# Kernel optimization log

Hardware: AMD Instinct MI355X
Metric: run time of the kernel (lower is better)

The kernel has to match this reference:

```python
import jax, jax.numpy as jnp
import numpy as np

N_NODES = 100000
N_EDGES = 600000
IN_SIZE = 128
OUT_SIZE = 128
N_GRAPHS = 100
BN_EPS = 1e-5


def setup_inputs() -> dict:
    key = jax.random.key(0)
    ks = jax.random.split(key, 8)
    h = jax.random.normal(ks[0], (N_NODES, IN_SIZE), dtype=jnp.float32)
    norm = jax.random.uniform(ks[1], (N_NODES, 1), dtype=jnp.float32)
    src = jax.random.randint(ks[2], (N_EDGES,), 0, N_NODES, dtype=jnp.int32)
    dst = jax.random.randint(ks[3], (N_EDGES,), 0, N_NODES, dtype=jnp.int32)
    graph_ids = jnp.sort(jax.random.randint(ks[4], (N_NODES,), 0, N_GRAPHS, dtype=jnp.int32))
    # Linear + BatchNorm params
    W = jax.random.normal(ks[5], (IN_SIZE, OUT_SIZE), dtype=jnp.float32) / np.sqrt(IN_SIZE)
    b = jnp.zeros((OUT_SIZE,), dtype=jnp.float32)
    gamma = jnp.ones((OUT_SIZE,), dtype=jnp.float32)
    beta = jnp.zeros((OUT_SIZE,), dtype=jnp.float32)
    return {"h": h, "norm": norm, "W": W, "b": b, "gamma": gamma, "beta": beta,
            "src": src, "dst": dst, "graph_ids": graph_ids}


def reference(h, norm, W, b, gamma, beta, src, dst, graph_ids):
    # pre-normalize, scatter-sum over edges (copy_src + sum), post-normalize
    x = h * norm                                            # [N, in]
    agg = jax.ops.segment_sum(x[src], dst, num_segments=N_NODES)  # SpMM
    x = agg * norm
    # linear + relu
    x = jax.nn.relu(jnp.dot(x, W) + b)                      # [N, out]
    # BatchNorm1d (training-mode: batch mean, biased variance)
    mean = jnp.mean(x, axis=0)
    var = jnp.mean(jnp.square(x - mean), axis=0)
    x = (x - mean) * jax.lax.rsqrt(var + BN_EPS) * gamma + beta
    # sum_nodes pooling per graph
    phis = jax.ops.segment_sum(x, graph_ids, num_segments=N_GRAPHS)  # [G, out]
    return (x, phis)
```

## Files before the change

kernel.cpp:

```cpp
#include <hip/hip_runtime.h>
#include <hip/hip_bf16.h>

#define N_NODES 100000
#define N_EDGES 600000
#define CH 128
#define N_GRAPHS 100
#define BN_EPS 1e-5f
#define NBUCKET 32
#define CAP 16
#define OVFCAP 8192
#define EDGE_BLOCKS 2344
#define GEMM_BLOCKS 1563
#define GATHER_BLOCKS 2048
#define BN_BLOCKS 1563
#define ZERO_INTS (N_NODES + 2 * NBUCKET * CH + 4)
#define ZERO_BLOCKS 423
#define PHIS_BLOCKS 50
#define WT_BLOCKS 64

typedef __bf16 bf16x8 __attribute__((ext_vector_type(8)));
typedef float f32x4 __attribute__((ext_vector_type(4)));

__device__ __forceinline__ ushort f2bf(float f) {
    union { float f; unsigned u; } x; x.f = f;
    unsigned u = x.u;
    unsigned r = (u + 0x7fffu + ((u >> 16) & 1u)) >> 16;
    return (ushort)r;
}
__device__ __forceinline__ float bflo(unsigned p) { return __builtin_bit_cast(float, p << 16); }
__device__ __forceinline__ float bfhi(unsigned p) { return __builtin_bit_cast(float, p & 0xffff0000u); }

__global__ __launch_bounds__(256) void k_prep(const float* __restrict__ W,
        int* __restrict__ zbase, ushort* __restrict__ Wt, float* __restrict__ phis) {
    unsigned bid = blockIdx.x;
    int tid = threadIdx.x;
    if (bid < ZERO_BLOCKS) {
        int i = bid * 256 + tid;
        if (i < ZERO_INTS) zbase[i] = 0;
    } else if (bid < ZERO_BLOCKS + PHIS_BLOCKS) {
        int i = (bid - ZERO_BLOCKS) * 256 + tid;
        phis[i] = 0.f;
    } else {
        int t = (bid - ZERO_BLOCKS - PHIS_BLOCKS) * 256 + tid;
        int k = t >> 7, o = t & 127;
        Wt[o * CH + k] = f2bf(W[t]);
    }
}

__global__ __launch_bounds__(256) void k_fill(const int* __restrict__ src,
        const int* __restrict__ dst, int* __restrict__ cnt,
        int* __restrict__ ovfcur, int* __restrict__ ovf, int* __restrict__ esrc) {
    int e = blockIdx.x * 256 + threadIdx.x;
    if (e < N_EDGES) {
        int d = dst[e], s = src[e];
        int slot = atomicAdd(&cnt[d], 1);
        if (slot < CAP) esrc[d * CAP + slot] = s;
        else { int p = atomicAdd(ovfcur, 1); if (p < OVFCAP) { ovf[2*p] = d; ovf[2*p+1] = s; } }
    }
}

__device__ __forceinline__ bf16x8 mk_b(const float* __restrict__ hrow, int k,
                                       float nm, bool valid) {
    union { bf16x8 v; ushort u[8]; } r;
    if (valid) {
        float4 p = *(const float4*)(hrow + k);
        float4 q = *(const float4*)(hrow + k + 4);
        r.u[0] = f2bf(p.x * nm); r.u[1] = f2bf(p.y * nm);
        r.u[2] = f2bf(p.z * nm); r.u[3] = f2bf(p.w * nm);
        r.u[4] = f2bf(q.x * nm); r.u[5] = f2bf(q.y * nm);
        r.u[6] = f2bf(q.z * nm); r.u[7] = f2bf(q.w * nm);
    } else {
        #pragma unroll
        for (int i = 0; i < 8; i++) r.u[i] = 0;
    }
    return r.v;
}

__global__ __launch_bounds__(256) void k_zgemm(const float* __restrict__ h,
        const float* __restrict__ norm, const ushort* __restrict__ Wt,
        ushort* __restrict__ z16) {
    int tid = threadIdx.x;
    int w = tid >> 6, L = tid & 63;
    int c15 = L & 15, quad = L >> 4;
    int n0 = blockIdx.x * 64 + w * 16 + c15;
    bool v0 = n0 < N_NODES;
    float nm0 = v0 ? norm[n0] : 0.f;
    const float* h0 = h + (size_t)n0 * CH;

    f32x4 acc[8] = {};
    #pragma unroll
    for (int kt = 0; kt < 4; kt++) {
        int k = kt * 32 + quad * 8;
        bf16x8 b0 = mk_b(h0, k, nm0, v0);
        #pragma unroll
        for (int ot = 0; ot < 8; ot++) {
            bf16x8 a = *(const bf16x8*)(Wt + (size_t)(ot * 16 + c15) * CH + k);
            acc[ot] = __builtin_amdgcn_mfma_f32_16x16x32_bf16(a, b0, acc[ot], 0, 0, 0);
        }
    }

    if (v0) {
        ushort* zr = z16 + (size_t)n0 * CH;
        #pragma unroll
        for (int ot = 0; ot < 8; ot++) {
            uint2 dv;
            dv.x = (unsigned)f2bf(acc[ot][0]) | ((unsigned)f2bf(acc[ot][1]) << 16);
            dv.y = (unsigned)f2bf(acc[ot][2]) | ((unsigned)f2bf(acc[ot][3]) << 16);
            *(uint2*)(zr + ot * 16 + quad * 4) = dv;
        }
    }
}

__global__ __launch_bounds__(256) void k_gather(const ushort* __restrict__ z16,
        const float* __restrict__ norm, const int* __restrict__ cnt,
        const int* __restrict__ esrc, const int* __restrict__ ovfcur,
        const int* __restrict__ ovf, const float* __restrict__ bias,
        ushort* __restrict__ y16, float* __restrict__ psum, float* __restrict__ psq) {
    __shared__ float sred[2][16][CH];

    int tid = threadIdx.x;
    int cg = tid & 15, rl = tid >> 4;
    int c = cg * 8;
    float4 b0 = *(const float4*)(bias + c), b1 = *(const float4*)(bias + c + 4);
    float s8[8] = {}, q8[8] = {};
    int no = min(*ovfcur, OVFCAP);

    for (int n = blockIdx.x * 16 + rl; n < N_NODES; n += GATHER_BLOCKS * 16) {
        int craw = cnt[n];
        int e = min(craw, CAP);
        float nn = norm[n];
        int base = n * CAP;
        float a0=0.f,a1=0.f,a2=0.f,a3=0.f,a4=0.f,a5=0.f,a6=0.f,a7=0.f;
        int j = 0;
        for (; j + 4 <= e; j += 4) {
            int4 s4 = *(const int4*)(esrc + base + j);
            uint4 v0 = *(const uint4*)(z16 + (size_t)s4.x * CH + c);
            uint4 v1 = *(const uint4*)(z16 + (size_t)s4.y * CH + c);
            uint4 v2 = *(const uint4*)(z16 + (size_t)s4.z * CH + c);
            uint4 v3 = *(const uint4*)(z16 + (size_t)s4.w * CH + c);
            a0 += bflo(v0.x) + bflo(v1.x) + bflo(v2.x) + bflo(v3.x);
            a1 += bfhi(v0.x) + bfhi(v1.x) + bfhi(v2.x) + bfhi(v3.x);
            a2 += bflo(v0.y) + bflo(v1.y) + bflo(v2.y) + bflo(v3.y);
            a3 += bfhi(v0.y) + bfhi(v1.y) + bfhi(v2.y) + bfhi(v3.y);
            a4 += bflo(v0.z) + bflo(v1.z) + bflo(v2.z) + bflo(v3.z);
            a5 += bfhi(v0.z) + bfhi(v1.z) + bfhi(v2.z) + bfhi(v3.z);
            a6 += bflo(v0.w) + bflo(v1.w) + bflo(v2.w) + bflo(v3.w);
            a7 += bfhi(v0.w) + bfhi(v1.w) + bfhi(v2.w) + bfhi(v3.w);
        }
        for (; j < e; j++) {
            int s = esrc[base + j];
            uint4 v = *(const uint4*)(z16 + (size_t)s * CH + c);
            a0 += bflo(v.x); a1 += bfhi(v.x);
            a2 += bflo(v.y); a3 += bfhi(v.y);
            a4 += bflo(v.z); a5 += bfhi(v.z);
            a6 += bflo(v.w); a7 += bfhi(v.w);
        }
        if (craw > CAP && no > 0) {
            for (int i = 0; i < no; i++) {
                if (ovf[2*i] == n) {
                    int s = ovf[2*i+1];
                    uint4 v = *(const uint4*)(z16 + (size_t)s * CH + c);
                    a0 += bflo(v.x); a1 += bfhi(v.x);
                    a2 += bflo(v.y); a3 += bfhi(v.y);
                    a4 += bflo(v.z); a5 += bfhi(v.z);
                    a6 += bflo(v.w); a7 += bfhi(v.w);
                }
            }
        }
        float f[8];
        f[0] = fmaxf(fmaf(a0, nn, b0.x), 0.f);
        f[1] = fmaxf(fmaf(a1, nn, b0.y), 0.f);
        f[2] = fmaxf(fmaf(a2, nn, b0.z), 0.f);
        f[3] = fmaxf(fmaf(a3, nn, b0.w), 0.f);
        f[4] = fmaxf(fmaf(a4, nn, b1.x), 0.f);
        f[5] = fmaxf(fmaf(a5, nn, b1.y), 0.f);
        f[6] = fmaxf(fmaf(a6, nn, b1.z), 0.f);
        f[7] = fmaxf(fmaf(a7, nn, b1.w), 0.f);
        uint4 o;
        o.x = (unsigned)f2bf(f[0]) | ((unsigned)f2bf(f[1]) << 16);
        o.y = (unsigned)f2bf(f[2]) | ((unsigned)f2bf(f[3]) << 16);
        o.z = (unsigned)f2bf(f[4]) | ((unsigned)f2bf(f[5]) << 16);
        o.w = (unsigned)f2bf(f[6]) | ((unsigned)f2bf(f[7]) << 16);
        *(uint4*)(y16 + (size_t)n * CH + c) = o;
        #pragma unroll
        for (int k = 0; k < 8; k++) { s8[k] += f[k]; q8[k] += f[k] * f[k]; }
    }

    *(float4*)&sred[0][rl][c]     = make_float4(s8[0], s8[1], s8[2], s8[3]);
    *(float4*)&sred[0][rl][c + 4] = make_float4(s8[4], s8[5], s8[6], s8[7]);
    *(float4*)&sred[1][rl][c]     = make_float4(q8[0], q8[1], q8[2], q8[3]);
    *(float4*)&sred[1][rl][c + 4] = make_float4(q8[4], q8[5], q8[6], q8[7]);
    __syncthreads();
    if (tid < 128) {
        float S = 0.f, Q = 0.f;
        #pragma unroll
        for (int k = 0; k < 16; k++) { S += sred[0][k][tid]; Q += sred[1][k][tid]; }
        int bucket = blockIdx.x & (NBUCKET - 1);
        atomicAdd(&psum[bucket * CH + tid], S);
        atomicAdd(&psq[bucket * CH + tid], Q);
    }
}

__global__ __launch_bounds__(256) void k_bnpool(const ushort* __restrict__ y16,
        const int* __restrict__ gids, const float* __restrict__ psum,
        const float* __restrict__ psq, const float* __restrict__ gamma,
        const float* __restrict__ beta, float* __restrict__ xout,
        float* __restrict__ phis) {
    __shared__ float smP[16][CH];
    __shared__ float ssc[CH], ssh[CH];

    int tid = threadIdx.x;
    if (tid < 128) {
        float S = 0.f, Q = 0.f;
        #pragma unroll
        for (int g = 0; g < NBUCKET; g++) { S += psum[g * CH + tid]; Q += psq[g * CH + tid]; }
        const float invN = 1.f / (float)N_NODES;
        float mean = S * invN;
        float var  = Q * invN - mean * mean;
        float sc   = gamma[tid] * rsqrtf(var + BN_EPS);
        ssc[tid] = sc;
        ssh[tid] = beta[tid] - mean * sc;
    }
    __syncthreads();

    int cg = tid & 15, rl = tid >> 4;
    int c = cg * 8;
    int r0 = blockIdx.x * 64;
    int rbase = r0 + rl * 4;

    float4 sc0 = *(const float4*)&ssc[c], sc1 = *(const float4*)&ssc[c + 4];
    float4 sh0 = *(const float4*)&ssh[c], sh1 = *(const float4*)&ssh[c + 4];

    bool fast = (r0 + 63 < N_NODES) && (gids[r0] == gids[r0 + 63]);

    if (fast) {
        float4 p0 = make_float4(0.f,0.f,0.f,0.f), p1 = make_float4(0.f,0.f,0.f,0.f);
        #pragma unroll
        for (int j = 0; j < 4; j++) {
            int r = rbase + j;
            uint4 v = *(const uint4*)(y16 + (size_t)r * CH + c);
            float4 f0, f1;
            f0.x = fmaf(bflo(v.x), sc0.x, sh0.x); f0.y = fmaf(bfhi(v.x), sc0.y, sh0.y);
            f0.z = fmaf(bflo(v.y), sc0.z, sh0.z); f0.w = fmaf(bfhi(v.y), sc0.w, sh0.w);
            f1.x = fmaf(bflo(v.z), sc1.x, sh1.x); f1.y = fmaf(bfhi(v.z), sc1.y, sh1.y);
            f1.z = fmaf(bflo(v.w), sc1.z, sh1.z); f1.w = fmaf(bfhi(v.w), sc1.w, sh1.w);
            *(float4*)(xout + (size_t)r * CH + c) = f0;
            *(float4*)(xout + (size_t)r * CH + c + 4) = f1;
            p0.x += f0.x; p0.y += f0.y; p0.z += f0.z; p0.w += f0.w;
            p1.x += f1.x; p1.y += f1.y; p1.z += f1.z; p1.w += f1.w;
        }
        *(float4*)&smP[rl][c] = p0;
        *(float4*)&smP[rl][c + 4] = p1;
        __syncthreads();
        if (tid < 128) {
            int g = gids[r0];
            float S = 0.f;
            #pragma unroll
            for (int k = 0; k < 16; k++) S += smP[k][tid];
            atomicAdd(&phis[(size_t)g * CH + tid], S);
        }
    } else {
        float p[8] = {};
        int gprev = -1;
        #pragma unroll
        for (int j = 0; j < 4; j++) {
            int r = rbase + j;
            if (r >= N_NODES) break;
            int g = gids[r];
            if (g != gprev) {
                if (gprev >= 0) {
                    #pragma unroll
                    for (int k = 0; k < 8; k++) {
                        atomicAdd(&phis[(size_t)gprev * CH + c + k], p[k]);
                        p[k] = 0.f;
                    }
                }
                gprev = g;
            }
            uint4 v = *(const uint4*)(y16 + (size_t)r * CH + c);
            float f[8];
            f[0] = fmaf(bflo(v.x), sc0.x, sh0.x); f[1] = fmaf(bfhi(v.x), sc0.y, sh0.y);
            f[2] = fmaf(bflo(v.y), sc0.z, sh0.z); f[3] = fmaf(bfhi(v.y), sc0.w, sh0.w);
            f[4] = fmaf(bflo(v.z), sc1.x, sh1.x); f[5] = fmaf(bfhi(v.z), sc1.y, sh1.y);
            f[6] = fmaf(bflo(v.w), sc1.z, sh1.z); f[7] = fmaf(bfhi(v.w), sc1.w, sh1.w);
            *(float4*)(xout + (size_t)r * CH + c) = make_float4(f[0], f[1], f[2], f[3]);
            *(float4*)(xout + (size_t)r * CH + c + 4) = make_float4(f[4], f[5], f[6], f[7]);
            #pragma unroll
            for (int k = 0; k < 8; k++) p[k] += f[k];
        }
        if (gprev >= 0) {
            #pragma unroll
            for (int k = 0; k < 8; k++)
                atomicAdd(&phis[(size_t)gprev * CH + c + k], p[k]);
        }
    }
}

extern "C" void kernel_launch(void* const* d_in, const int* in_sizes, int n_in,
                              void* d_out, int out_size, void* d_ws, size_t ws_size,
                              hipStream_t stream)
{
    const float* h     = (const float*)d_in[0];
    const float* norm  = (const float*)d_in[1];
    const float* W     = (const float*)d_in[2];
    const float* b     = (const float*)d_in[3];
    const float* gamma = (const float*)d_in[4];
    const float* beta  = (const float*)d_in[5];
    const int*   src   = (const int*)d_in[6];
    const int*   dst   = (const int*)d_in[7];
    const int*   gids  = (const int*)d_in[8];

    float* x_out = (float*)d_out;
    float* phis  = x_out + (size_t)N_NODES * CH;

    ushort* z16  = (ushort*)d_ws;
    ushort* y16  = z16 + (size_t)N_NODES * CH;
    ushort* Wt   = y16 + (size_t)N_NODES * CH;
    int*   cnt     = (int*)(Wt + CH * CH);
    float* psum    = (float*)(cnt + N_NODES);
    float* psq     = psum + NBUCKET * CH;
    int*   ovfcur  = (int*)(psq + NBUCKET * CH);
    int*   esrc    = ovfcur + 4;
    int*   ovf     = esrc + (size_t)N_NODES * CAP;

    k_prep<<<ZERO_BLOCKS + PHIS_BLOCKS + WT_BLOCKS, 256, 0, stream>>>(W, cnt, Wt, phis);
    k_fill<<<EDGE_BLOCKS, 256, 0, stream>>>(src, dst, cnt, ovfcur, ovf, esrc);
    k_zgemm<<<GEMM_BLOCKS, 256, 0, stream>>>(h, norm, Wt, z16);
    k_gather<<<GATHER_BLOCKS, 256, 0, stream>>>(
        z16, norm, cnt, esrc, ovfcur, ovf, b, y16, psum, psq);
    k_bnpool<<<BN_BLOCKS, 256, 0, stream>>>(
        y16, gids, psum, psq, gamma, beta, x_out, phis);
}
```

Baseline: 234.0 us.

## Hoist h loads in GEMM, defer norm scaling, split BN finalize into kernel

The GEMM kernel now issues all eight float4 loads of a node's h row up front, converts them to bf16, and applies the norm factor to the accumulator outputs instead of the inputs. This raises memory-level parallelism and cuts multiplies. The per-block BN statistics reduction in k_bnpool moves into a tiny single-block finalize kernel, so each of the 1563 blocks no longer re-reads 32 buckets. The esrc scatter store in k_fill becomes nontemporal. The cost is one extra launch, and rounding changes slightly because norm is applied after the bf16 product rather than before.

```diff
diff --git a/kernel.cpp b/kernel.cpp
--- a/kernel.cpp
+++ b/kernel.cpp
@@ -54,26 +54,9 @@
     if (e < N_EDGES) {
         int d = dst[e], s = src[e];
         int slot = atomicAdd(&cnt[d], 1);
-        if (slot < CAP) esrc[d * CAP + slot] = s;
+        if (slot < CAP) __builtin_nontemporal_store(s, &esrc[d * CAP + slot]);
         else { int p = atomicAdd(ovfcur, 1); if (p < OVFCAP) { ovf[2*p] = d; ovf[2*p+1] = s; } }
     }
-}
-
-__device__ __forceinline__ bf16x8 mk_b(const float* __restrict__ hrow, int k,
-                                       float nm, bool valid) {
-    union { bf16x8 v; ushort u[8]; } r;
-    if (valid) {
-        float4 p = *(const float4*)(hrow + k);
-        float4 q = *(const float4*)(hrow + k + 4);
-        r.u[0] = f2bf(p.x * nm); r.u[1] = f2bf(p.y * nm);
-        r.u[2] = f2bf(p.z * nm); r.u[3] = f2bf(p.w * nm);
-        r.u[4] = f2bf(q.x * nm); r.u[5] = f2bf(q.y * nm);
-        r.u[6] = f2bf(q.z * nm); r.u[7] = f2bf(q.w * nm);
-    } else {
-        #pragma unroll
-        for (int i = 0; i < 8; i++) r.u[i] = 0;
-    }
-    return r.v;
 }
 
 __global__ __launch_bounds__(256) void k_zgemm(const float* __restrict__ h,
@@ -84,18 +67,35 @@
     int c15 = L & 15, quad = L >> 4;
     int n0 = blockIdx.x * 64 + w * 16 + c15;
     bool v0 = n0 < N_NODES;
+    int nr = v0 ? n0 : 0;
+    const float* h0 = h + (size_t)nr * CH;
     float nm0 = v0 ? norm[n0] : 0.f;
-    const float* h0 = h + (size_t)n0 * CH;
+
+    float4 hv[8];
+    #pragma unroll
+    for (int i = 0; i < 8; i++)
+        hv[i] = *(const float4*)(h0 + (i >> 1) * 32 + quad * 8 + (i & 1) * 4);
+
+    bf16x8 bfr[4];
+    #pragma unroll
+    for (int kt = 0; kt < 4; kt++) {
+        union { bf16x8 v; ushort u[8]; } r;
+        float4 p = hv[2 * kt], q = hv[2 * kt + 1];
+        r.u[0] = f2bf(p.x); r.u[1] = f2bf(p.y);
+        r.u[2] = f2bf(p.z); r.u[3] = f2bf(p.w);
+        r.u[4] = f2bf(q.x); r.u[5] = f2bf(q.y);
+        r.u[6] = f2bf(q.z); r.u[7] = f2bf(q.w);
+        bfr[kt] = r.v;
+    }
 
     f32x4 acc[8] = {};
     #pragma unroll
     for (int kt = 0; kt < 4; kt++) {
         int k = kt * 32 + quad * 8;
-        bf16x8 b0 = mk_b(h0, k, nm0, v0);
         #pragma unroll
         for (int ot = 0; ot < 8; ot++) {
             bf16x8 a = *(const bf16x8*)(Wt + (size_t)(ot * 16 + c15) * CH + k);
-            acc[ot] = __builtin_amdgcn_mfma_f32_16x16x32_bf16(a, b0, acc[ot], 0, 0, 0);
+            acc[ot] = __builtin_amdgcn_mfma_f32_16x16x32_bf16(a, bfr[kt], acc[ot], 0, 0, 0);
         }
     }
 
@@ -103,9 +103,11 @@
         ushort* zr = z16 + (size_t)n0 * CH;
         #pragma unroll
         for (int ot = 0; ot < 8; ot++) {
+            float z0 = acc[ot][0] * nm0, z1 = acc[ot][1] * nm0;
+            float z2 = acc[ot][2] * nm0, z3 = acc[ot][3] * nm0;
             uint2 dv;
-            dv.x = (unsigned)f2bf(acc[ot][0]) | ((unsigned)f2bf(acc[ot][1]) << 16);
-            dv.y = (unsigned)f2bf(acc[ot][2]) | ((unsigned)f2bf(acc[ot][3]) << 16);
+            dv.x = (unsigned)f2bf(z0) | ((unsigned)f2bf(z1) << 16);
+            dv.y = (unsigned)f2bf(z2) | ((unsigned)f2bf(z3) << 16);
             *(uint2*)(zr + ot * 16 + quad * 4) = dv;
         }
     }
@@ -201,35 +203,35 @@
     }
 }
 
+__global__ void k_finalize(const float* __restrict__ psum, const float* __restrict__ psq,
+        const float* __restrict__ gamma, const float* __restrict__ beta,
+        float* __restrict__ scale, float* __restrict__ shift) {
+    int t = threadIdx.x;
+    float S = 0.f, Q = 0.f;
+    #pragma unroll
+    for (int g = 0; g < NBUCKET; g++) { S += psum[g * CH + t]; Q += psq[g * CH + t]; }
+    const float invN = 1.f / (float)N_NODES;
+    float mean = S * invN;
+    float var  = Q * invN - mean * mean;
+    float sc   = gamma[t] * rsqrtf(var + BN_EPS);
+    scale[t] = sc;
+    shift[t] = beta[t] - mean * sc;
+}
+
 __global__ __launch_bounds__(256) void k_bnpool(const ushort* __restrict__ y16,
-        const int* __restrict__ gids, const float* __restrict__ psum,
-        const float* __restrict__ psq, const float* __restrict__ gamma,
-        const float* __restrict__ beta, float* __restrict__ xout,
+        const int* __restrict__ gids, const float* __restrict__ scale,
+        const float* __restrict__ shift, float* __restrict__ xout,
         float* __restrict__ phis) {
     __shared__ float smP[16][CH];
-    __shared__ float ssc[CH], ssh[CH];
 
     int tid = threadIdx.x;
-    if (tid < 128) {
-        float S = 0.f, Q = 0.f;
-        #pragma unroll
-        for (int g = 0; g < NBUCKET; g++) { S += psum[g * CH + tid]; Q += psq[g * CH + tid]; }
-        const float invN = 1.f / (float)N_NODES;
-        float mean = S * invN;
-        float var  = Q * invN - mean * mean;
-        float sc   = gamma[tid] * rsqrtf(var + BN_EPS);
-        ssc[tid] = sc;
-        ssh[tid] = beta[tid] - mean * sc;
-    }
-    __syncthreads();
-
     int cg = tid & 15, rl = tid >> 4;
     int c = cg * 8;
     int r0 = blockIdx.x * 64;
     int rbase = r0 + rl * 4;
 
-    float4 sc0 = *(const float4*)&ssc[c], sc1 = *(const float4*)&ssc[c + 4];
-    float4 sh0 = *(const float4*)&ssh[c], sh1 = *(const float4*)&ssh[c + 4];
+    float4 sc0 = *(const float4*)(scale + c), sc1 = *(const float4*)(scale + c + 4);
+    float4 sh0 = *(const float4*)(shift + c), sh1 = *(const float4*)(shift + c + 4);
 
     bool fast = (r0 + 63 < N_NODES) && (gids[r0] == gids[r0 + 63]);
 
@@ -322,12 +324,15 @@
     int*   ovfcur  = (int*)(psq + NBUCKET * CH);
     int*   esrc    = ovfcur + 4;
     int*   ovf     = esrc + (size_t)N_NODES * CAP;
+    float* scale   = (float*)(ovf + 2 * OVFCAP);
+    float* shift   = scale + CH;
 
     k_prep<<<ZERO_BLOCKS + PHIS_BLOCKS + WT_BLOCKS, 256, 0, stream>>>(W, cnt, Wt, phis);
     k_fill<<<EDGE_BLOCKS, 256, 0, stream>>>(src, dst, cnt, ovfcur, ovf, esrc);
     k_zgemm<<<GEMM_BLOCKS, 256, 0, stream>>>(h, norm, Wt, z16);
     k_gather<<<GATHER_BLOCKS, 256, 0, stream>>>(
         z16, norm, cnt, esrc, ovfcur, ovf, b, y16, psum, psq);
+    k_finalize<<<1, 128, 0, stream>>>(psum, psq, gamma, beta, scale, shift);
     k_bnpool<<<BN_BLOCKS, 256, 0, stream>>>(
-        y16, gids, psum, psq, gamma, beta, x_out, phis);
-}
+        y16, gids, scale, shift, x_out, phis);
+}
```

Result: slower. 242.6 us (+3.7%).
